# Performance work log

Hardware: AMD Instinct MI355X
Metric: run time of the kernel (lower is better)

Reference implementation:

```python
import jax, jax.numpy as jnp
import numpy as np

B, L, E, D1, D2 = 256, 128, 64, 512, 512


def setup_inputs() -> dict:
    key = jax.random.key(0)
    k1, k2, k3, kw = jax.random.split(key, 4)
    tensor1 = jax.random.normal(k1, (B, L, D1), dtype=jnp.float32)
    tensor2 = jax.random.normal(k2, (B, L, D2), dtype=jnp.float32)
    parameters_index = jax.random.randint(k3, (B,), 0, E, dtype=jnp.int32)
    # xavier_uniform with relu gain: gain*sqrt(6/(fan_in+fan_out)),
    # torch fan for [E,D1,D2]: fan_in = D1*D2, fan_out = E*D2
    gain = float(np.sqrt(2.0))
    bound = gain * float(np.sqrt(6.0 / (D1 * D2 + E * D2)))
    weights = jax.random.uniform(kw, (E, D1, D2), minval=-bound, maxval=bound, dtype=jnp.float32)
    return {"tensor1": tensor1, "tensor2": tensor2, "parameters_index": parameters_index, "weights": weights}


def reference(tensor1, tensor2, parameters_index, weights):
    # gather per-batch weight matrix [B, D1, D2], then bilinear form x1^T W x2
    w = weights[parameters_index]  # [B, D1, D2]
    # equals: sum over i,j of tensor1[b,l,i] * w[b,i,j] * tensor2[b,l,j] -> [B, L]
    return jnp.einsum('bli,bij,blj->bl', tensor1, w, tensor2)
```

## Files before the change

### kernel.cpp

```cpp
#include <hip/hip_runtime.h>
#include <stdint.h>

#define NB 256
#define NL 128
#define ND1 512
#define ND2 512
#define NE 64

#define BI 128
#define BK 64
#define NKT (ND2 / BK)
#define LDST 72
#define BUFSZ ((NL + BI) * LDST)

typedef float float4_t __attribute__((ext_vector_type(4)));
typedef __bf16 bf16x8_t __attribute__((ext_vector_type(8)));
typedef unsigned short ushort4_t __attribute__((ext_vector_type(4)));
typedef unsigned short ushort8_t __attribute__((ext_vector_type(8)));

__device__ __forceinline__ unsigned short f2bf(float f) {
    unsigned int u = __float_as_uint(f);
    u += 0x7FFFu + ((u >> 16) & 1u);
    return (unsigned short)(u >> 16);
}

__device__ __forceinline__ ushort4_t cvt4(float4_t v) {
    ushort4_t u;
    u.x = f2bf(v.x); u.y = f2bf(v.y); u.z = f2bf(v.z); u.w = f2bf(v.w);
    return u;
}

__global__ void pre_kernel(const int* __restrict__ pidx, int* __restrict__ perm,
                           float* __restrict__ out, int zero_n, int do_sort)
{
    const int g = blockIdx.x, t = threadIdx.x;
    const int idx = g * 256 + t;
    if (idx < zero_n) out[idx] = 0.f;
    if (do_sort && g == 0) {
        __shared__ int cnt[NE];
        __shared__ int base[NE];
        if (t < NE) cnt[t] = 0;
        __syncthreads();
        const int e = pidx[t];
        const int r = atomicAdd(&cnt[e], 1);
        __syncthreads();
        if (t == 0) {
            int s = 0;
            for (int i = 0; i < NE; ++i) { base[i] = s; s += cnt[i]; }
        }
        __syncthreads();
        perm[base[e] + r] = t;
    }
}

template <bool USE_PERM>
__global__ __launch_bounds__(512, 4) void pdot_kernel(
    const float* __restrict__ t1, const float* __restrict__ t2,
    const int* __restrict__ pidx, const float* __restrict__ wgt,
    const int* __restrict__ perm, float* __restrict__ out)
{
    __shared__ unsigned short sm[2][BUFSZ];

    const int g  = blockIdx.x;
    const int x  = g & 7;
    const int s  = g >> 3;
    const int slot = x * 32 + (s >> 2);
    const int b  = USE_PERM ? perm[slot] : slot;
    const int it = s & 3;
    const int i0 = it * BI;

    const int t  = threadIdx.x;
    const int w  = t >> 6;
    const int wv = w & 3;
    const int ih = w >> 2;
    const int ln = t & 63;
    const int nh = ln & 15;
    const int qd = ln >> 4;

    const int e = pidx[b];
    const float* aPtr = t2  + (size_t)b * (NL * ND2);
    const float* bPtr = wgt + (size_t)e * (ND1 * ND2) + (size_t)i0 * ND2;
    const float* t1p  = t1  + (size_t)b * (NL * ND1) + i0 + ih * 64;

    float4_t acc[2][4];
    #pragma unroll
    for (int i = 0; i < 2; ++i)
        #pragma unroll
        for (int j = 0; j < 4; ++j) {
            float4_t z = {0.f, 0.f, 0.f, 0.f};
            acc[i][j] = z;
        }

    const int s_row = t >> 4;
    const int s_kq  = (t & 15) * 4;
    const size_t sOff = (size_t)s_row * ND2 + s_kq;
    const int wOff  = s_row * LDST + s_kq;
    const int wOffB = (NL + s_row) * LDST + s_kq;

    float4_t pa[4], pb[4];

    #pragma unroll
    for (int p = 0; p < 4; ++p) {
        pa[p] = *(const float4_t*)(aPtr + sOff + (size_t)p * (32 * ND2));
        pb[p] = *(const float4_t*)(bPtr + sOff + (size_t)p * (32 * ND2));
    }
    #pragma unroll
    for (int p = 0; p < 4; ++p) {
        *(ushort4_t*)(&sm[0][wOff  + p * (32 * LDST)]) = cvt4(pa[p]);
        *(ushort4_t*)(&sm[0][wOffB + p * (32 * LDST)]) = cvt4(pb[p]);
    }
    #pragma unroll
    for (int p = 0; p < 4; ++p) {
        pa[p] = *(const float4_t*)(aPtr + sOff + BK + (size_t)p * (32 * ND2));
        pb[p] = *(const float4_t*)(bPtr + sOff + BK + (size_t)p * (32 * ND2));
    }
    __builtin_amdgcn_sched_barrier(0);
    asm volatile("s_waitcnt lgkmcnt(0)" ::: "memory");
    __builtin_amdgcn_sched_barrier(0);
    __builtin_amdgcn_s_barrier();
    __builtin_amdgcn_sched_barrier(0);

    #pragma unroll
    for (int kt = 0; kt < NKT; ++kt) {
        const int cur = kt & 1;
        const int nxt = cur ^ 1;
        const unsigned short* cA = &sm[cur][0];
        const unsigned short* cB = &sm[cur][NL * LDST];

        {
            const int kf = qd * 8;
            const int ra = wv * 32 + nh;
            bf16x8_t af0 = __builtin_bit_cast(bf16x8_t, *(const ushort8_t*)(&cA[(ra     ) * LDST + kf]));
            bf16x8_t af1 = __builtin_bit_cast(bf16x8_t, *(const ushort8_t*)(&cA[(ra + 16) * LDST + kf]));
            bf16x8_t bv[4];
            #pragma unroll
            for (int ns = 0; ns < 4; ++ns)
                bv[ns] = __builtin_bit_cast(bf16x8_t, *(const ushort8_t*)(&cB[(ih * 64 + ns * 16 + nh) * LDST + kf]));
            __builtin_amdgcn_s_setprio(1);
            #pragma unroll
            for (int ns = 0; ns < 4; ++ns) {
                acc[0][ns] = __builtin_amdgcn_mfma_f32_16x16x32_bf16(af0, bv[ns], acc[0][ns], 0, 0, 0);
                acc[1][ns] = __builtin_amdgcn_mfma_f32_16x16x32_bf16(af1, bv[ns], acc[1][ns], 0, 0, 0);
            }
            __builtin_amdgcn_s_setprio(0);
        }

        if (kt < NKT - 1) {
            #pragma unroll
            for (int p = 0; p < 4; ++p)
                *(ushort4_t*)(&sm[nxt][wOff + p * (32 * LDST)]) = cvt4(pa[p]);
        }

        {
            const int kf = 32 + qd * 8;
            const int ra = wv * 32 + nh;
            bf16x8_t af0 = __builtin_bit_cast(bf16x8_t, *(const ushort8_t*)(&cA[(ra     ) * LDST + kf]));
            bf16x8_t af1 = __builtin_bit_cast(bf16x8_t, *(const ushort8_t*)(&cA[(ra + 16) * LDST + kf]));
            bf16x8_t bv[4];
            #pragma unroll
            for (int ns = 0; ns < 4; ++ns)
                bv[ns] = __builtin_bit_cast(bf16x8_t, *(const ushort8_t*)(&cB[(ih * 64 + ns * 16 + nh) * LDST + kf]));
            __builtin_amdgcn_s_setprio(1);
            #pragma unroll
            for (int ns = 0; ns < 4; ++ns) {
                acc[0][ns] = __builtin_amdgcn_mfma_f32_16x16x32_bf16(af0, bv[ns], acc[0][ns], 0, 0, 0);
                acc[1][ns] = __builtin_amdgcn_mfma_f32_16x16x32_bf16(af1, bv[ns], acc[1][ns], 0, 0, 0);
            }
            __builtin_amdgcn_s_setprio(0);
        }

        if (kt < NKT - 1) {
            #pragma unroll
            for (int p = 0; p < 4; ++p)
                *(ushort4_t*)(&sm[nxt][wOffB + p * (32 * LDST)]) = cvt4(pb[p]);
            if (kt < NKT - 2) {
                const size_t k0 = (size_t)(kt + 2) * BK;
                #pragma unroll
                for (int p = 0; p < 4; ++p) {
                    pa[p] = *(const float4_t*)(aPtr + sOff + k0 + (size_t)p * (32 * ND2));
                    pb[p] = *(const float4_t*)(bPtr + sOff + k0 + (size_t)p * (32 * ND2));
                }
                __builtin_amdgcn_sched_barrier(0);
            }
            asm volatile("s_waitcnt lgkmcnt(0)" ::: "memory");
            __builtin_amdgcn_sched_barrier(0);
            __builtin_amdgcn_s_barrier();
            __builtin_amdgcn_sched_barrier(0);
        }
    }

    #pragma unroll
    for (int ms = 0; ms < 2; ++ms) {
        #pragma unroll
        for (int r = 0; r < 4; ++r) {
            const int row = wv * 32 + ms * 16 + qd * 4 + r;
            float ps = 0.f;
            #pragma unroll
            for (int ns = 0; ns < 4; ++ns) {
                const float tv = t1p[(size_t)row * ND1 + ns * 16 + nh];
                ps += acc[ms][ns][r] * tv;
            }
            ps += __shfl_xor(ps, 1);
            ps += __shfl_xor(ps, 2);
            ps += __shfl_xor(ps, 4);
            ps += __shfl_xor(ps, 8);
            if (nh == 0) atomicAdd(&out[b * NL + row], ps);
        }
    }
}

extern "C" void kernel_launch(void* const* d_in, const int* in_sizes, int n_in,
                              void* d_out, int out_size, void* d_ws, size_t ws_size,
                              hipStream_t stream)
{
    const float* t1  = (const float*)d_in[0];
    const float* t2  = (const float*)d_in[1];
    const int* pidx  = (const int*)d_in[2];
    const float* wgt = (const float*)d_in[3];
    float* out = (float*)d_out;

    const int zero_blocks = (out_size + 255) / 256;
    const bool have_ws = ws_size >= NB * sizeof(int);
    int* perm = have_ws ? (int*)d_ws : nullptr;

    pre_kernel<<<dim3(zero_blocks), dim3(256), 0, stream>>>(pidx, perm, out, out_size, have_ws ? 1 : 0);

    if (have_ws)
        pdot_kernel<true><<<dim3(NB * (ND1 / BI)), dim3(512), 0, stream>>>(t1, t2, pidx, wgt, perm, out);
    else
        pdot_kernel<false><<<dim3(NB * (ND1 / BI)), dim3(512), 0, stream>>>(t1, t2, pidx, wgt, nullptr, out);
}
```

Measured before the change: 207.6 us.

## Load tensor2 fragments directly from global into registers, stage only weights in LDS

The tensor2 (A operand) tile is no longer staged through shared memory. Each wave loads its MFMA A fragments straight from global memory, converts them to bf16 in registers and prefetches one k-substep ahead. Only the weight tile is double-buffered in LDS, and the K tile grows from 64 to 128, which halves the number of barriers per block. The cost is that the A fragment loads are strided, uncoalesced global reads that the two wave-groups (ih) each read redundantly, and the larger in-flight weight prefetch raises register pressure.

```diff
diff --git a/kernel.cpp b/kernel.cpp
--- a/kernel.cpp
+++ b/kernel.cpp
@@ -8,10 +8,9 @@
 #define NE 64
 
 #define BI 128
-#define BK 64
+#define BK 128
 #define NKT (ND2 / BK)
-#define LDST 72
-#define BUFSZ ((NL + BI) * LDST)
+#define LDSTB 136
 
 typedef float float4_t __attribute__((ext_vector_type(4)));
 typedef __bf16 bf16x8_t __attribute__((ext_vector_type(8)));
@@ -28,6 +27,13 @@
     ushort4_t u;
     u.x = f2bf(v.x); u.y = f2bf(v.y); u.z = f2bf(v.z); u.w = f2bf(v.w);
     return u;
+}
+
+__device__ __forceinline__ bf16x8_t cvt8(float4_t a, float4_t b) {
+    ushort8_t u;
+    u[0] = f2bf(a.x); u[1] = f2bf(a.y); u[2] = f2bf(a.z); u[3] = f2bf(a.w);
+    u[4] = f2bf(b.x); u[5] = f2bf(b.y); u[6] = f2bf(b.z); u[7] = f2bf(b.w);
+    return __builtin_bit_cast(bf16x8_t, u);
 }
 
 __global__ void pre_kernel(const int* __restrict__ pidx, int* __restrict__ perm,
@@ -59,7 +65,7 @@
     const int* __restrict__ pidx, const float* __restrict__ wgt,
     const int* __restrict__ perm, float* __restrict__ out)
 {
-    __shared__ unsigned short sm[2][BUFSZ];
+    __shared__ unsigned short sB[2][BI * LDSTB];
 
     const int g  = blockIdx.x;
     const int x  = g & 7;
@@ -82,6 +88,9 @@
     const float* bPtr = wgt + (size_t)e * (ND1 * ND2) + (size_t)i0 * ND2;
     const float* t1p  = t1  + (size_t)b * (NL * ND1) + i0 + ih * 64;
 
+    const float* aF0 = aPtr + (size_t)(wv * 32 + nh) * ND2 + qd * 8;
+    const float* aF1 = aF0 + (size_t)16 * ND2;
+
     float4_t acc[2][4];
     #pragma unroll
     for (int i = 0; i < 2; ++i)
@@ -91,29 +100,22 @@
             acc[i][j] = z;
         }
 
-    const int s_row = t >> 4;
-    const int s_kq  = (t & 15) * 4;
-    const size_t sOff = (size_t)s_row * ND2 + s_kq;
-    const int wOff  = s_row * LDST + s_kq;
-    const int wOffB = (NL + s_row) * LDST + s_kq;
-
-    float4_t pa[4], pb[4];
-
-    #pragma unroll
-    for (int p = 0; p < 4; ++p) {
-        pa[p] = *(const float4_t*)(aPtr + sOff + (size_t)p * (32 * ND2));
-        pb[p] = *(const float4_t*)(bPtr + sOff + (size_t)p * (32 * ND2));
-    }
-    #pragma unroll
-    for (int p = 0; p < 4; ++p) {
-        *(ushort4_t*)(&sm[0][wOff  + p * (32 * LDST)]) = cvt4(pa[p]);
-        *(ushort4_t*)(&sm[0][wOffB + p * (32 * LDST)]) = cvt4(pb[p]);
-    }
-    #pragma unroll
-    for (int p = 0; p < 4; ++p) {
-        pa[p] = *(const float4_t*)(aPtr + sOff + BK + (size_t)p * (32 * ND2));
-        pb[p] = *(const float4_t*)(bPtr + sOff + BK + (size_t)p * (32 * ND2));
-    }
+    const int r_row = t >> 5;
+    const int c4    = (t & 31) * 4;
+    const size_t bOff = (size_t)r_row * ND2 + c4;
+    const int wOffB = r_row * LDSTB + c4;
+
+    float4_t pb[8];
+
+    #pragma unroll
+    for (int p = 0; p < 8; ++p)
+        pb[p] = *(const float4_t*)(bPtr + bOff + (size_t)p * (16 * ND2));
+    #pragma unroll
+    for (int p = 0; p < 8; ++p)
+        *(ushort4_t*)(&sB[0][wOffB + p * (16 * LDSTB)]) = cvt4(pb[p]);
+    #pragma unroll
+    for (int p = 0; p < 8; ++p)
+        pb[p] = *(const float4_t*)(bPtr + bOff + BK + (size_t)p * (16 * ND2));
     __builtin_amdgcn_sched_barrier(0);
     asm volatile("s_waitcnt lgkmcnt(0)" ::: "memory");
     __builtin_amdgcn_sched_barrier(0);
@@ -124,18 +126,30 @@
     for (int kt = 0; kt < NKT; ++kt) {
         const int cur = kt & 1;
         const int nxt = cur ^ 1;
-        const unsigned short* cA = &sm[cur][0];
-        const unsigned short* cB = &sm[cur][NL * LDST];
-
-        {
-            const int kf = qd * 8;
-            const int ra = wv * 32 + nh;
-            bf16x8_t af0 = __builtin_bit_cast(bf16x8_t, *(const ushort8_t*)(&cA[(ra     ) * LDST + kf]));
-            bf16x8_t af1 = __builtin_bit_cast(bf16x8_t, *(const ushort8_t*)(&cA[(ra + 16) * LDST + kf]));
+        const unsigned short* cB = &sB[cur][0];
+        const int kbase = kt * BK;
+
+        float4_t a00 = *(const float4_t*)(aF0 + kbase);
+        float4_t a01 = *(const float4_t*)(aF0 + kbase + 4);
+        float4_t a10 = *(const float4_t*)(aF1 + kbase);
+        float4_t a11 = *(const float4_t*)(aF1 + kbase + 4);
+
+        #pragma unroll
+        for (int ks = 0; ks < 4; ++ks) {
+            const int kf = ks * 32 + qd * 8;
             bf16x8_t bv[4];
             #pragma unroll
             for (int ns = 0; ns < 4; ++ns)
-                bv[ns] = __builtin_bit_cast(bf16x8_t, *(const ushort8_t*)(&cB[(ih * 64 + ns * 16 + nh) * LDST + kf]));
+                bv[ns] = __builtin_bit_cast(bf16x8_t, *(const ushort8_t*)(&cB[(ih * 64 + ns * 16 + nh) * LDSTB + kf]));
+            bf16x8_t af0 = cvt8(a00, a01);
+            bf16x8_t af1 = cvt8(a10, a11);
+            if (ks < 3) {
+                const int kn = kbase + (ks + 1) * 32;
+                a00 = *(const float4_t*)(aF0 + kn);
+                a01 = *(const float4_t*)(aF0 + kn + 4);
+                a10 = *(const float4_t*)(aF1 + kn);
+                a11 = *(const float4_t*)(aF1 + kn + 4);
+            }
             __builtin_amdgcn_s_setprio(1);
             #pragma unroll
             for (int ns = 0; ns < 4; ++ns) {
@@ -143,45 +157,28 @@
                 acc[1][ns] = __builtin_amdgcn_mfma_f32_16x16x32_bf16(af1, bv[ns], acc[1][ns], 0, 0, 0);
             }
             __builtin_amdgcn_s_setprio(0);
-        }
-
+
+            if (kt < NKT - 1) {
+                if (ks == 1) {
+                    #pragma unroll
+                    for (int p = 0; p < 4; ++p)
+                        *(ushort4_t*)(&sB[nxt][wOffB + p * (16 * LDSTB)]) = cvt4(pb[p]);
+                } else if (ks == 2) {
+                    #pragma unroll
+                    for (int p = 4; p < 8; ++p)
+                        *(ushort4_t*)(&sB[nxt][wOffB + p * (16 * LDSTB)]) = cvt4(pb[p]);
+                }
+            }
+        }
+
+        if (kt < NKT - 2) {
+            const size_t k0 = (size_t)(kt + 2) * BK;
+            #pragma unroll
+            for (int p = 0; p < 8; ++p)
+                pb[p] = *(const float4_t*)(bPtr + bOff + k0 + (size_t)p * (16 * ND2));
+            __builtin_amdgcn_sched_barrier(0);
+        }
         if (kt < NKT - 1) {
-            #pragma unroll
-            for (int p = 0; p < 4; ++p)
-                *(ushort4_t*)(&sm[nxt][wOff + p * (32 * LDST)]) = cvt4(pa[p]);
-        }
-
-        {
-            const int kf = 32 + qd * 8;
-            const int ra = wv * 32 + nh;
-            bf16x8_t af0 = __builtin_bit_cast(bf16x8_t, *(const ushort8_t*)(&cA[(ra     ) * LDST + kf]));
-            bf16x8_t af1 = __builtin_bit_cast(bf16x8_t, *(const ushort8_t*)(&cA[(ra + 16) * LDST + kf]));
-            bf16x8_t bv[4];
-            #pragma unroll
-            for (int ns = 0; ns < 4; ++ns)
-                bv[ns] = __builtin_bit_cast(bf16x8_t, *(const ushort8_t*)(&cB[(ih * 64 + ns * 16 + nh) * LDST + kf]));
-            __builtin_amdgcn_s_setprio(1);
-            #pragma unroll
-            for (int ns = 0; ns < 4; ++ns) {
-                acc[0][ns] = __builtin_amdgcn_mfma_f32_16x16x32_bf16(af0, bv[ns], acc[0][ns], 0, 0, 0);
-                acc[1][ns] = __builtin_amdgcn_mfma_f32_16x16x32_bf16(af1, bv[ns], acc[1][ns], 0, 0, 0);
-            }
-            __builtin_amdgcn_s_setprio(0);
-        }
-
-        if (kt < NKT - 1) {
-            #pragma unroll
-            for (int p = 0; p < 4; ++p)
-                *(ushort4_t*)(&sm[nxt][wOffB + p * (32 * LDST)]) = cvt4(pb[p]);
-            if (kt < NKT - 2) {
-                const size_t k0 = (size_t)(kt + 2) * BK;
-                #pragma unroll
-                for (int p = 0; p < 4; ++p) {
-                    pa[p] = *(const float4_t*)(aPtr + sOff + k0 + (size_t)p * (32 * ND2));
-                    pb[p] = *(const float4_t*)(bPtr + sOff + k0 + (size_t)p * (32 * ND2));
-                }
-                __builtin_amdgcn_sched_barrier(0);
-            }
             asm volatile("s_waitcnt lgkmcnt(0)" ::: "memory");
             __builtin_amdgcn_sched_barrier(0);
             __builtin_amdgcn_s_barrier();
```

Result: slower. 232.1 us (+11.8%).

## Use 4 waves per block with 32x128 warp tiles and BK=32

Applied to the files above, without the earlier changes.

Halves the block to 256 threads (4 waves), with each wave now covering all 128 output columns (8 N-subtiles) instead of 64. This doubles accumulator registers and lets each A fragment feed twice as many MFMAs. The K step shrinks from 64 to 32, with LDS padding reduced to match, so there are twice as many barrier-synchronised iterations with smaller staging per iteration. The aim is to reduce A-fragment LDS reads and lower per-block thread count. The cost is more barriers, more register pressure and less latency hiding per block.

```diff
diff --git a/kernel.cpp b/kernel.cpp
--- a/kernel.cpp
+++ b/kernel.cpp
@@ -8,9 +8,9 @@
 #define NE 64
 
 #define BI 128
-#define BK 64
+#define BK 32
 #define NKT (ND2 / BK)
-#define LDST 72
+#define LDST 40
 #define BUFSZ ((NL + BI) * LDST)
 
 typedef float float4_t __attribute__((ext_vector_type(4)));
@@ -54,7 +54,7 @@
 }
 
 template <bool USE_PERM>
-__global__ __launch_bounds__(512, 4) void pdot_kernel(
+__global__ __launch_bounds__(256, 4) void pdot_kernel(
     const float* __restrict__ t1, const float* __restrict__ t2,
     const int* __restrict__ pidx, const float* __restrict__ wgt,
     const int* __restrict__ perm, float* __restrict__ out)
@@ -70,9 +70,7 @@
     const int i0 = it * BI;
 
     const int t  = threadIdx.x;
-    const int w  = t >> 6;
-    const int wv = w & 3;
-    const int ih = w >> 2;
+    const int wv = t >> 6;
     const int ln = t & 63;
     const int nh = ln & 15;
     const int qd = ln >> 4;
@@ -80,22 +78,22 @@
     const int e = pidx[b];
     const float* aPtr = t2  + (size_t)b * (NL * ND2);
     const float* bPtr = wgt + (size_t)e * (ND1 * ND2) + (size_t)i0 * ND2;
-    const float* t1p  = t1  + (size_t)b * (NL * ND1) + i0 + ih * 64;
-
-    float4_t acc[2][4];
+    const float* t1p  = t1  + (size_t)b * (NL * ND1) + i0;
+
+    float4_t acc[2][8];
     #pragma unroll
     for (int i = 0; i < 2; ++i)
         #pragma unroll
-        for (int j = 0; j < 4; ++j) {
+        for (int j = 0; j < 8; ++j) {
             float4_t z = {0.f, 0.f, 0.f, 0.f};
             acc[i][j] = z;
         }
 
-    const int s_row = t >> 4;
-    const int s_kq  = (t & 15) * 4;
-    const size_t sOff = (size_t)s_row * ND2 + s_kq;
-    const int wOff  = s_row * LDST + s_kq;
-    const int wOffB = (NL + s_row) * LDST + s_kq;
+    const int s_row = t >> 3;
+    const int s_c4  = (t & 7) * 4;
+    const size_t sOff = (size_t)s_row * ND2 + s_c4;
+    const int wOffA = s_row * LDST + s_c4;
+    const int wOffB = (NL + s_row) * LDST + s_c4;
 
     float4_t pa[4], pb[4];
 
@@ -106,7 +104,7 @@
     }
     #pragma unroll
     for (int p = 0; p < 4; ++p) {
-        *(ushort4_t*)(&sm[0][wOff  + p * (32 * LDST)]) = cvt4(pa[p]);
+        *(ushort4_t*)(&sm[0][wOffA + p * (32 * LDST)]) = cvt4(pa[p]);
         *(ushort4_t*)(&sm[0][wOffB + p * (32 * LDST)]) = cvt4(pb[p]);
     }
     #pragma unroll
@@ -127,52 +125,29 @@
         const unsigned short* cA = &sm[cur][0];
         const unsigned short* cB = &sm[cur][NL * LDST];
 
-        {
-            const int kf = qd * 8;
-            const int ra = wv * 32 + nh;
-            bf16x8_t af0 = __builtin_bit_cast(bf16x8_t, *(const ushort8_t*)(&cA[(ra     ) * LDST + kf]));
-            bf16x8_t af1 = __builtin_bit_cast(bf16x8_t, *(const ushort8_t*)(&cA[(ra + 16) * LDST + kf]));
-            bf16x8_t bv[4];
-            #pragma unroll
-            for (int ns = 0; ns < 4; ++ns)
-                bv[ns] = __builtin_bit_cast(bf16x8_t, *(const ushort8_t*)(&cB[(ih * 64 + ns * 16 + nh) * LDST + kf]));
-            __builtin_amdgcn_s_setprio(1);
-            #pragma unroll
-            for (int ns = 0; ns < 4; ++ns) {
-                acc[0][ns] = __builtin_amdgcn_mfma_f32_16x16x32_bf16(af0, bv[ns], acc[0][ns], 0, 0, 0);
-                acc[1][ns] = __builtin_amdgcn_mfma_f32_16x16x32_bf16(af1, bv[ns], acc[1][ns], 0, 0, 0);
-            }
-            __builtin_amdgcn_s_setprio(0);
-        }
+        const int kf = qd * 8;
+        const int ra = wv * 32 + nh;
+        bf16x8_t af0 = __builtin_bit_cast(bf16x8_t, *(const ushort8_t*)(&cA[(ra     ) * LDST + kf]));
+        bf16x8_t af1 = __builtin_bit_cast(bf16x8_t, *(const ushort8_t*)(&cA[(ra + 16) * LDST + kf]));
+        bf16x8_t bv[8];
+        #pragma unroll
+        for (int ns = 0; ns < 8; ++ns)
+            bv[ns] = __builtin_bit_cast(bf16x8_t, *(const ushort8_t*)(&cB[(ns * 16 + nh) * LDST + kf]));
+
+        __builtin_amdgcn_s_setprio(1);
+        #pragma unroll
+        for (int ns = 0; ns < 8; ++ns) {
+            acc[0][ns] = __builtin_amdgcn_mfma_f32_16x16x32_bf16(af0, bv[ns], acc[0][ns], 0, 0, 0);
+            acc[1][ns] = __builtin_amdgcn_mfma_f32_16x16x32_bf16(af1, bv[ns], acc[1][ns], 0, 0, 0);
+        }
+        __builtin_amdgcn_s_setprio(0);
 
         if (kt < NKT - 1) {
             #pragma unroll
-            for (int p = 0; p < 4; ++p)
-                *(ushort4_t*)(&sm[nxt][wOff + p * (32 * LDST)]) = cvt4(pa[p]);
-        }
-
-        {
-            const int kf = 32 + qd * 8;
-            const int ra = wv * 32 + nh;
-            bf16x8_t af0 = __builtin_bit_cast(bf16x8_t, *(const ushort8_t*)(&cA[(ra     ) * LDST + kf]));
-            bf16x8_t af1 = __builtin_bit_cast(bf16x8_t, *(const ushort8_t*)(&cA[(ra + 16) * LDST + kf]));
-            bf16x8_t bv[4];
-            #pragma unroll
-            for (int ns = 0; ns < 4; ++ns)
-                bv[ns] = __builtin_bit_cast(bf16x8_t, *(const ushort8_t*)(&cB[(ih * 64 + ns * 16 + nh) * LDST + kf]));
-            __builtin_amdgcn_s_setprio(1);
-            #pragma unroll
-            for (int ns = 0; ns < 4; ++ns) {
-                acc[0][ns] = __builtin_amdgcn_mfma_f32_16x16x32_bf16(af0, bv[ns], acc[0][ns], 0, 0, 0);
-                acc[1][ns] = __builtin_amdgcn_mfma_f32_16x16x32_bf16(af1, bv[ns], acc[1][ns], 0, 0, 0);
+            for (int p = 0; p < 4; ++p) {
+                *(ushort4_t*)(&sm[nxt][wOffA + p * (32 * LDST)]) = cvt4(pa[p]);
+                *(ushort4_t*)(&sm[nxt][wOffB + p * (32 * LDST)]) = cvt4(pb[p]);
             }
-            __builtin_amdgcn_s_setprio(0);
-        }
-
-        if (kt < NKT - 1) {
-            #pragma unroll
-            for (int p = 0; p < 4; ++p)
-                *(ushort4_t*)(&sm[nxt][wOffB + p * (32 * LDST)]) = cvt4(pb[p]);
             if (kt < NKT - 2) {
                 const size_t k0 = (size_t)(kt + 2) * BK;
                 #pragma unroll
@@ -196,7 +171,7 @@
             const int row = wv * 32 + ms * 16 + qd * 4 + r;
             float ps = 0.f;
             #pragma unroll
-            for (int ns = 0; ns < 4; ++ns) {
+            for (int ns = 0; ns < 8; ++ns) {
                 const float tv = t1p[(size_t)row * ND1 + ns * 16 + nh];
                 ps += acc[ms][ns][r] * tv;
             }
@@ -226,7 +201,7 @@
     pre_kernel<<<dim3(zero_blocks), dim3(256), 0, stream>>>(pidx, perm, out, out_size, have_ws ? 1 : 0);
 
     if (have_ws)
-        pdot_kernel<true><<<dim3(NB * (ND1 / BI)), dim3(512), 0, stream>>>(t1, t2, pidx, wgt, perm, out);
+        pdot_kernel<true><<<dim3(NB * (ND1 / BI)), dim3(256), 0, stream>>>(t1, t2, pidx, wgt, perm, out);
     else
-        pdot_kernel<false><<<dim3(NB * (ND1 / BI)), dim3(512), 0, stream>>>(t1, t2, pidx, wgt, nullptr, out);
-}
+        pdot_kernel<false><<<dim3(NB * (ND1 / BI)), dim3(256), 0, stream>>>(t1, t2, pidx, wgt, nullptr, out);
+}
```

Result: slower. 349.0 us (+68.1%).
